# Performance work log

Measured on AMD Instinct MI355X. Metric: run time of the kernel, lower is better.

## Reference

```python
import jax, jax.numpy as jnp
import numpy as np

EPS = 1e-6


def setup_inputs() -> dict:
    key = jax.random.key(0)
    k1, k2, k3 = jax.random.split(key, 3)
    h, w, K = 480, 640, 21
    n = h * w
    segmentation = jax.random.uniform(k1, (n, K), dtype=jnp.float32)  # per-pixel plane probs in (0,1)
    prob = jax.random.uniform(k2, (n, 1), dtype=jnp.float32)
    gt_instance = jax.random.randint(k3, (21, h, w), 0, 2, dtype=jnp.int32)  # binary GT masks
    return {
        "segmentation": segmentation,
        "prob": prob,
        "gt_instance": gt_instance,
        "gt_plane_num": 20,
    }


def reference(segmentation, prob, gt_instance, gt_plane_num):
    # segmentation: (N, K) probabilities; gt_instance: (21, h, w) binary; gt_plane_num: python int
    n, k = segmentation.shape
    # (G, N) float masks for the first gt_plane_num GT instances
    gi = gt_instance[:gt_plane_num].reshape(gt_plane_num, -1).astype(jnp.float32)
    seg = segmentation.T  # (K, N)
    log_p = jnp.log(seg + EPS)        # (K, N)
    log_1p = jnp.log(1.0 - seg + EPS)  # (K, N)
    # mean over pixels of -(gi*log_p + (1-gi)*log_1p), expressed as two GEMMs
    # instead of materializing the (K, G, N) broadcast tensor:
    # ce[k, g] = -( sum_n log_p[k,n]*gi[g,n] + sum_n log_1p[k,n]*(1-gi[g,n]) ) / N
    inv_n = jnp.float32(1.0 / n)
    ce = -(log_p @ gi.T + log_1p @ (1.0 - gi).T) * inv_n  # (K, G)
    matching = jnp.argmin(ce, axis=1, keepdims=True)  # (K, 1) int
    return matching
```

## Files before the change

### kernel.cpp

```cpp
#include <hip/hip_runtime.h>

#define EPSF 1e-6f
#define TPB 256
#define KMAXC 21
#define NGR 21
#define RW 72
#define SLICE (KMAXC * RW)
#define TBL 1024
#define MAXBLK 1152

typedef float  f32x4  __attribute__((ext_vector_type(4)));
typedef float  f32x16 __attribute__((ext_vector_type(16)));
typedef __bf16 bf16x8 __attribute__((ext_vector_type(8)));
typedef __bf16 bf16x4 __attribute__((ext_vector_type(4)));

struct GroupRegs { f32x4 s[6]; int4 g[6]; };

__device__ __forceinline__ void issue_loads(const float* __restrict__ seg,
                                            const int* __restrict__ gt,
                                            int N, int GROWS, int p0, int lane,
                                            GroupRegs& r) {
    const f32x4* s4 = (const f32x4*)(seg + (size_t)p0 * KMAXC);
    #pragma unroll
    for (int q = 0; q < 6; ++q) {
        const int i4 = lane + (q << 6);
        f32x4 v = {0.5f, 0.5f, 0.5f, 0.5f};
        if (i4 < 336) v = s4[i4];
        r.s[q] = v;
    }
    #pragma unroll
    for (int q = 0; q < 6; ++q) {
        const int i4 = lane + (q << 6);
        int4 gv = {0, 0, 0, 0};
        if (i4 < 336) {
            int row = i4 >> 4;
            row = (row < GROWS) ? row : (GROWS - 1);
            gv = *(const int4*)(gt + (size_t)row * N + p0 + ((i4 & 15) << 2));
        }
        r.g[q] = gv;
    }
}

__device__ __forceinline__ void scatter_group(__bf16* dl, __bf16* ml, int lane,
                                              const GroupRegs& r) {
    #pragma unroll
    for (int q = 0; q < 6; ++q) {
        const int i4 = lane + (q << 6);
        if (i4 < 336) {
            const int lin = i4 << 2;
            int pix = lin / KMAXC;
            int k   = lin - pix * KMAXC;
            #pragma unroll
            for (int c = 0; c < 4; ++c) {
                const float s = r.s[q][c];
                const float dd = __log2f(s + EPSF) - __log2f(1.0f - s + EPSF);
                dl[k * RW + pix] = (__bf16)dd;
                if (++k == KMAXC) { k = 0; ++pix; }
            }
            const int row = i4 >> 4;
            bf16x4 mv;
            mv[0] = (__bf16)(float)(r.g[q].x != 0);
            mv[1] = (__bf16)(float)(r.g[q].y != 0);
            mv[2] = (__bf16)(float)(r.g[q].z != 0);
            mv[3] = (__bf16)(float)(r.g[q].w != 0);
            *(bf16x4*)(ml + row * RW + ((i4 & 15) << 2)) = mv;
        }
    }
}

__device__ __forceinline__ void mfma_group(const __bf16* dl, const __bf16* ml,
                                           int lane, int K, f32x16& acc) {
    const int r31  = lane & 31;
    const int rowA = (r31 < K)   ? r31 : (K - 1);
    const int rowB = (r31 < NGR) ? r31 : (NGR - 1);
    const int off  = (lane >> 5) << 3;
    const __bf16* pa = dl + rowA * RW + off;
    const __bf16* pb = ml + rowB * RW + off;
    #pragma unroll
    for (int i = 0; i < 4; ++i) {
        const bf16x8 af = *(const bf16x8*)(pa + i * 16);
        const bf16x8 bf = *(const bf16x8*)(pb + i * 16);
        acc = __builtin_amdgcn_mfma_f32_32x32x16_bf16(af, bf, acc, 0, 0, 0);
    }
}

__device__ __forceinline__ void generic_group(const float* __restrict__ seg,
                                              const int* __restrict__ gt,
                                              __bf16* dl, __bf16* ml, int lane,
                                              int N, int K, int GROWS, int p0) {
    for (int i = lane; i < K * 64; i += 64) {
        const int pix = i / K, k = i - pix * K;
        const float s = (p0 + pix < N) ? seg[(size_t)(p0 + pix) * K + k] : 0.5f;
        const float dd = __log2f(s + EPSF) - __log2f(1.0f - s + EPSF);
        if (k < KMAXC) dl[k * RW + pix] = (__bf16)dd;
    }
    for (int i = lane; i < NGR * 64; i += 64) {
        const int row = i >> 6, c = i & 63;
        int val = 0;
        if (row < GROWS && p0 + c < N) val = (gt[(size_t)row * N + p0 + c] != 0);
        ml[row * RW + c] = (__bf16)(float)val;
    }
}

__global__ __launch_bounds__(TPB) void msk_main(
    const float* __restrict__ seg,
    const int* __restrict__ gt,
    float* __restrict__ sums,
    int N, int K, int GROWS, int NGROUP, int NBLK)
{
    const int tid  = threadIdx.x;
    const int lane = tid & 63;
    const int wv   = tid >> 6;

    __shared__ union {
        __bf16 stage[4][2][SLICE];
        float  red[4 * TBL];
    } u;

    f32x16 acc = {};
    __bf16* dl = u.stage[wv][0];
    __bf16* ml = u.stage[wv][1];

    const int W  = NBLK * 4;
    const int gw = (int)blockIdx.x * 4 + wv;

    if (K == KMAXC) {
        const int g0 = gw, g1 = gw + W;
        const bool f0 = (g0 < NGROUP) && ((g0 << 6) + 64 <= N);
        const bool f1 = (g1 < NGROUP) && ((g1 << 6) + 64 <= N);
        GroupRegs r0, r1;
        if (f0) issue_loads(seg, gt, N, GROWS, g0 << 6, lane, r0);
        if (f1) issue_loads(seg, gt, N, GROWS, g1 << 6, lane, r1);
        if (f0) { scatter_group(dl, ml, lane, r0); mfma_group(dl, ml, lane, K, acc); }
        if (f1) { scatter_group(dl, ml, lane, r1); mfma_group(dl, ml, lane, K, acc); }
        if (g0 < NGROUP && !f0) {
            generic_group(seg, gt, dl, ml, lane, N, K, GROWS, g0 << 6);
            mfma_group(dl, ml, lane, K, acc);
        }
        if (g1 < NGROUP && !f1) {
            generic_group(seg, gt, dl, ml, lane, N, K, GROWS, g1 << 6);
            mfma_group(dl, ml, lane, K, acc);
        }
        for (int gid = gw + 2 * W; gid < NGROUP; gid += W) {
            const int p0 = gid << 6;
            if (p0 + 64 <= N) {
                GroupRegs r;
                issue_loads(seg, gt, N, GROWS, p0, lane, r);
                scatter_group(dl, ml, lane, r);
            } else {
                generic_group(seg, gt, dl, ml, lane, N, K, GROWS, p0);
            }
            mfma_group(dl, ml, lane, K, acc);
        }
    } else {
        for (int gid = gw; gid < NGROUP; gid += W) {
            generic_group(seg, gt, dl, ml, lane, N, K, GROWS, gid << 6);
            mfma_group(dl, ml, lane, K, acc);
        }
    }

    __syncthreads();
    {
        const int col = lane & 31;
        const int rhi = (lane >> 5) << 2;
        #pragma unroll
        for (int r = 0; r < 16; ++r) {
            const int row = (r & 3) + ((r >> 2) << 3) + rhi;
            u.red[wv * TBL + row * 32 + col] = acc[r];
        }
    }
    __syncthreads();

    {
        float* stbl = sums + (size_t)blockIdx.x * TBL;
        const int live = K * 32;
        for (int cell = tid; cell < live; cell += TPB) {
            const float v = u.red[cell] + u.red[TBL + cell]
                          + u.red[2 * TBL + cell] + u.red[3 * TBL + cell];
            __hip_atomic_store(&stbl[cell], v, __ATOMIC_RELAXED,
                               __HIP_MEMORY_SCOPE_AGENT);
        }
    }
}

__global__ __launch_bounds__(1024) void msk_final(
    const float* __restrict__ sums,
    const int* __restrict__ gpn,
    int* __restrict__ out,
    int K, int NBLK)
{
    const int G = *gpn;
    const int k = blockIdx.x;
    const int tid = threadIdx.x;
    const int col = tid & 31;
    const int grp = tid >> 5;

    const int tpg = NBLK >> 5;
    const int t0  = grp * tpg;
    const size_t rowoff = (size_t)k * 32 + col;

    #define AL(T) __hip_atomic_load(&sums[(size_t)(T) * TBL + rowoff], \
                                    __ATOMIC_RELAXED, __HIP_MEMORY_SCOPE_AGENT)
    float v0 = 0.f, v1 = 0.f, v2 = 0.f, v3 = 0.f;
    float v4 = 0.f, v5 = 0.f, v6 = 0.f, v7 = 0.f;
    int i = 0;
    for (; i + 8 <= tpg; i += 8) {
        v0 += AL(t0 + i + 0); v1 += AL(t0 + i + 1);
        v2 += AL(t0 + i + 2); v3 += AL(t0 + i + 3);
        v4 += AL(t0 + i + 4); v5 += AL(t0 + i + 5);
        v6 += AL(t0 + i + 6); v7 += AL(t0 + i + 7);
    }
    for (; i < tpg; ++i) v0 += AL(t0 + i);
    if (grp < (NBLK & 31)) v1 += AL((NBLK & ~31) + grp);
    #undef AL
    const float vv = ((v0 + v1) + (v2 + v3)) + ((v4 + v5) + (v6 + v7));

    __shared__ float P[32][33];
    __shared__ float A[32];
    P[grp][col] = vv;
    __syncthreads();
    if (tid < 32) {
        float s = 0.f;
        #pragma unroll
        for (int g2 = 0; g2 < 32; ++g2) s += P[g2][tid];
        A[tid] = s;
    }
    __syncthreads();

    if (tid == 0) {
        const int GG = (G < 32) ? G : 32;
        float bv; int bg = 0;
        if (GG > 0) {
            bv = A[0];
            for (int g = 1; g < GG; ++g) {
                const float v = A[g];
                if (v > bv) { bv = v; bg = g; }
            }
        }
        out[k] = bg;
    }
}

extern "C" void kernel_launch(void* const* d_in, const int* in_sizes, int n_in,
                              void* d_out, int out_size, void* d_ws, size_t ws_size,
                              hipStream_t stream) {
    const float* seg = (const float*)d_in[0];
    const int* gt  = (const int*)d_in[2];
    const int* gpn = (const int*)d_in[3];

    const int N = in_sizes[1];
    const int K = in_sizes[0] / N;
    const int GROWS = in_sizes[2] / N;
    const int NGROUP = (N + 63) >> 6;

    int NBLK = MAXBLK;
    const int minb = (NGROUP + 3) >> 2;
    if (NBLK > minb) NBLK = minb;
    const long long wcap = (long long)(ws_size / (TBL * sizeof(float)));
    if (NBLK > wcap) NBLK = (int)wcap;
    if (NBLK < 1) NBLK = 1;

    msk_main <<<NBLK, TPB, 0, stream>>>(seg, gt, (float*)d_ws,
                                        N, K, GROWS, NGROUP, NBLK);
    msk_final<<<K, 1024, 0, stream>>>((const float*)d_ws, gpn, (int*)d_out,
                                      K, NBLK);
}
```

Measured before the change: 22.16 us.

## Load GT mask MFMA fragments directly from global memory into registers

The binary GT mask B-operand is now built straight in registers from global int4 loads, packed into bf16 fragments with bit tricks, instead of being staged through LDS. This removes the mask LDS writes and reads and halves per-wave shared staging. The two-group software prefetch is dropped in favour of a single uniform loop, so less memory latency may be hidden. Each lane now loads one GT row's pixels matching the MFMA layout, which may give less coalesced global access.

```diff
diff --git a/kernel.cpp b/kernel.cpp
--- a/kernel.cpp
+++ b/kernel.cpp
@@ -3,7 +3,6 @@
 #define EPSF 1e-6f
 #define TPB 256
 #define KMAXC 21
-#define NGR 21
 #define RW 72
 #define SLICE (KMAXC * RW)
 #define TBL 1024
@@ -12,94 +11,18 @@
 typedef float  f32x4  __attribute__((ext_vector_type(4)));
 typedef float  f32x16 __attribute__((ext_vector_type(16)));
 typedef __bf16 bf16x8 __attribute__((ext_vector_type(8)));
-typedef __bf16 bf16x4 __attribute__((ext_vector_type(4)));
-
-struct GroupRegs { f32x4 s[6]; int4 g[6]; };
-
-__device__ __forceinline__ void issue_loads(const float* __restrict__ seg,
-                                            const int* __restrict__ gt,
-                                            int N, int GROWS, int p0, int lane,
-                                            GroupRegs& r) {
-    const f32x4* s4 = (const f32x4*)(seg + (size_t)p0 * KMAXC);
-    #pragma unroll
-    for (int q = 0; q < 6; ++q) {
-        const int i4 = lane + (q << 6);
-        f32x4 v = {0.5f, 0.5f, 0.5f, 0.5f};
-        if (i4 < 336) v = s4[i4];
-        r.s[q] = v;
-    }
-    #pragma unroll
-    for (int q = 0; q < 6; ++q) {
-        const int i4 = lane + (q << 6);
-        int4 gv = {0, 0, 0, 0};
-        if (i4 < 336) {
-            int row = i4 >> 4;
-            row = (row < GROWS) ? row : (GROWS - 1);
-            gv = *(const int4*)(gt + (size_t)row * N + p0 + ((i4 & 15) << 2));
-        }
-        r.g[q] = gv;
-    }
-}
-
-__device__ __forceinline__ void scatter_group(__bf16* dl, __bf16* ml, int lane,
-                                              const GroupRegs& r) {
-    #pragma unroll
-    for (int q = 0; q < 6; ++q) {
-        const int i4 = lane + (q << 6);
-        if (i4 < 336) {
-            const int lin = i4 << 2;
-            int pix = lin / KMAXC;
-            int k   = lin - pix * KMAXC;
-            #pragma unroll
-            for (int c = 0; c < 4; ++c) {
-                const float s = r.s[q][c];
-                const float dd = __log2f(s + EPSF) - __log2f(1.0f - s + EPSF);
-                dl[k * RW + pix] = (__bf16)dd;
-                if (++k == KMAXC) { k = 0; ++pix; }
-            }
-            const int row = i4 >> 4;
-            bf16x4 mv;
-            mv[0] = (__bf16)(float)(r.g[q].x != 0);
-            mv[1] = (__bf16)(float)(r.g[q].y != 0);
-            mv[2] = (__bf16)(float)(r.g[q].z != 0);
-            mv[3] = (__bf16)(float)(r.g[q].w != 0);
-            *(bf16x4*)(ml + row * RW + ((i4 & 15) << 2)) = mv;
-        }
-    }
-}
-
-__device__ __forceinline__ void mfma_group(const __bf16* dl, const __bf16* ml,
-                                           int lane, int K, f32x16& acc) {
-    const int r31  = lane & 31;
-    const int rowA = (r31 < K)   ? r31 : (K - 1);
-    const int rowB = (r31 < NGR) ? r31 : (NGR - 1);
-    const int off  = (lane >> 5) << 3;
-    const __bf16* pa = dl + rowA * RW + off;
-    const __bf16* pb = ml + rowB * RW + off;
-    #pragma unroll
-    for (int i = 0; i < 4; ++i) {
-        const bf16x8 af = *(const bf16x8*)(pa + i * 16);
-        const bf16x8 bf = *(const bf16x8*)(pb + i * 16);
-        acc = __builtin_amdgcn_mfma_f32_32x32x16_bf16(af, bf, acc, 0, 0, 0);
-    }
-}
-
-__device__ __forceinline__ void generic_group(const float* __restrict__ seg,
-                                              const int* __restrict__ gt,
-                                              __bf16* dl, __bf16* ml, int lane,
-                                              int N, int K, int GROWS, int p0) {
-    for (int i = lane; i < K * 64; i += 64) {
-        const int pix = i / K, k = i - pix * K;
-        const float s = (p0 + pix < N) ? seg[(size_t)(p0 + pix) * K + k] : 0.5f;
-        const float dd = __log2f(s + EPSF) - __log2f(1.0f - s + EPSF);
-        if (k < KMAXC) dl[k * RW + pix] = (__bf16)dd;
-    }
-    for (int i = lane; i < NGR * 64; i += 64) {
-        const int row = i >> 6, c = i & 63;
-        int val = 0;
-        if (row < GROWS && p0 + c < N) val = (gt[(size_t)row * N + p0 + c] != 0);
-        ml[row * RW + c] = (__bf16)(float)val;
-    }
+
+__device__ __forceinline__ unsigned pk01(int lo, int hi) {
+    return (lo != 0 ? 0x3F80u : 0u) | (hi != 0 ? 0x3F800000u : 0u);
+}
+
+__device__ __forceinline__ bf16x8 mask_frag(const int4& a, const int4& b) {
+    union { unsigned w[4]; bf16x8 v; } u;
+    u.w[0] = pk01(a.x, a.y);
+    u.w[1] = pk01(a.z, a.w);
+    u.w[2] = pk01(b.x, b.y);
+    u.w[3] = pk01(b.z, b.w);
+    return u.v;
 }
 
 __global__ __launch_bounds__(TPB) void msk_main(
@@ -113,49 +36,92 @@
     const int wv   = tid >> 6;
 
     __shared__ union {
-        __bf16 stage[4][2][SLICE];
+        __bf16 stage[4][SLICE];
         float  red[4 * TBL];
     } u;
 
     f32x16 acc = {};
-    __bf16* dl = u.stage[wv][0];
-    __bf16* ml = u.stage[wv][1];
+    __bf16* dl = u.stage[wv];
 
     const int W  = NBLK * 4;
     const int gw = (int)blockIdx.x * 4 + wv;
 
-    if (K == KMAXC) {
-        const int g0 = gw, g1 = gw + W;
-        const bool f0 = (g0 < NGROUP) && ((g0 << 6) + 64 <= N);
-        const bool f1 = (g1 < NGROUP) && ((g1 << 6) + 64 <= N);
-        GroupRegs r0, r1;
-        if (f0) issue_loads(seg, gt, N, GROWS, g0 << 6, lane, r0);
-        if (f1) issue_loads(seg, gt, N, GROWS, g1 << 6, lane, r1);
-        if (f0) { scatter_group(dl, ml, lane, r0); mfma_group(dl, ml, lane, K, acc); }
-        if (f1) { scatter_group(dl, ml, lane, r1); mfma_group(dl, ml, lane, K, acc); }
-        if (g0 < NGROUP && !f0) {
-            generic_group(seg, gt, dl, ml, lane, N, K, GROWS, g0 << 6);
-            mfma_group(dl, ml, lane, K, acc);
-        }
-        if (g1 < NGROUP && !f1) {
-            generic_group(seg, gt, dl, ml, lane, N, K, GROWS, g1 << 6);
-            mfma_group(dl, ml, lane, K, acc);
-        }
-        for (int gid = gw + 2 * W; gid < NGROUP; gid += W) {
-            const int p0 = gid << 6;
-            if (p0 + 64 <= N) {
-                GroupRegs r;
-                issue_loads(seg, gt, N, GROWS, p0, lane, r);
-                scatter_group(dl, ml, lane, r);
-            } else {
-                generic_group(seg, gt, dl, ml, lane, N, K, GROWS, p0);
-            }
-            mfma_group(dl, ml, lane, K, acc);
-        }
-    } else {
-        for (int gid = gw; gid < NGROUP; gid += W) {
-            generic_group(seg, gt, dl, ml, lane, N, K, GROWS, gid << 6);
-            mfma_group(dl, ml, lane, K, acc);
+    const int r31   = lane & 31;
+    const int rowA  = (r31 < K) ? r31 : (K - 1);
+    const int rowM  = (r31 < GROWS) ? r31 : (GROWS - 1);
+    const int half8 = (lane >> 5) << 3;
+    const __bf16* pa = dl + rowA * RW + half8;
+
+    for (int gid = gw; gid < NGROUP; gid += W) {
+        const int p0 = gid << 6;
+        bf16x8 bfrag[4];
+
+        if (K == KMAXC && p0 + 64 <= N) {
+            const int* gb = gt + (size_t)rowM * N + p0 + half8;
+            const int4 m0 = *(const int4*)(gb +  0), m1 = *(const int4*)(gb +  4);
+            const int4 m2 = *(const int4*)(gb + 16), m3 = *(const int4*)(gb + 20);
+            const int4 m4 = *(const int4*)(gb + 32), m5 = *(const int4*)(gb + 36);
+            const int4 m6 = *(const int4*)(gb + 48), m7 = *(const int4*)(gb + 52);
+
+            f32x4 sreg[6];
+            const f32x4* s4 = (const f32x4*)(seg + (size_t)p0 * KMAXC);
+            #pragma unroll
+            for (int q = 0; q < 6; ++q) {
+                const int i4 = lane + (q << 6);
+                f32x4 v = {0.5f, 0.5f, 0.5f, 0.5f};
+                if (i4 < 336) v = s4[i4];
+                sreg[q] = v;
+            }
+
+            bfrag[0] = mask_frag(m0, m1);
+            bfrag[1] = mask_frag(m2, m3);
+            bfrag[2] = mask_frag(m4, m5);
+            bfrag[3] = mask_frag(m6, m7);
+
+            #pragma unroll
+            for (int q = 0; q < 6; ++q) {
+                const int i4 = lane + (q << 6);
+                if (i4 < 336) {
+                    const int lin = i4 << 2;
+                    int pix = lin / KMAXC;
+                    int k   = lin - pix * KMAXC;
+                    #pragma unroll
+                    for (int c = 0; c < 4; ++c) {
+                        const float s = sreg[q][c];
+                        const float dd = __log2f(s + EPSF) - __log2f(1.0f - s + EPSF);
+                        dl[k * RW + pix] = (__bf16)dd;
+                        if (++k == KMAXC) { k = 0; ++pix; }
+                    }
+                }
+            }
+        } else {
+            for (int i = lane; i < K * 64; i += 64) {
+                const int pix = i / K, k = i - pix * K;
+                const float s = (p0 + pix < N) ? seg[(size_t)(p0 + pix) * K + k] : 0.5f;
+                const float dd = __log2f(s + EPSF) - __log2f(1.0f - s + EPSF);
+                if (k < KMAXC) dl[k * RW + pix] = (__bf16)dd;
+            }
+            #pragma unroll
+            for (int i = 0; i < 4; ++i) {
+                unsigned w[4];
+                #pragma unroll
+                for (int e = 0; e < 4; ++e) {
+                    const int pA = p0 + 16 * i + half8 + 2 * e;
+                    const int va = (pA < N) ? gt[(size_t)rowM * N + pA] : 0;
+                    const int vb = (pA + 1 < N) ? gt[(size_t)rowM * N + pA + 1] : 0;
+                    w[e] = pk01(va, vb);
+                }
+                union { unsigned ww[4]; bf16x8 v; } cvt;
+                cvt.ww[0] = w[0]; cvt.ww[1] = w[1];
+                cvt.ww[2] = w[2]; cvt.ww[3] = w[3];
+                bfrag[i] = cvt.v;
+            }
+        }
+
+        #pragma unroll
+        for (int i = 0; i < 4; ++i) {
+            const bf16x8 af = *(const bf16x8*)(pa + i * 16);
+            acc = __builtin_amdgcn_mfma_f32_32x32x16_bf16(af, bfrag[i], acc, 0, 0, 0);
         }
     }
 
```

After: 20.86 us. 1.06x faster.
